# Performance work log

Hardware: AMD Instinct MI355X
Metric: run time of the kernel (lower is better)

Reference implementation:

```python
import jax, jax.numpy as jnp
from jax import lax
import numpy as np

_BN_SCALE = 1.0 / float(np.sqrt(1.0 + 1e-5))  # eval BN: running_mean=0, running_var=1
SEMANTIC_GROUPS = [
    ("head_spine", [0, 1, 2, 3, 20]),
    ("left_arm", [4, 5, 6, 7, 21, 22]),
    ("right_arm", [8, 9, 10, 11, 23, 24]),
    ("left_leg", [12, 13, 14, 15]),
    ("right_leg", [16, 17, 18, 19]),
]
_SKELETON_EDGES = [(3, 2), (2, 20), (20, 1), (1, 0), (20, 4), (4, 5), (5, 6), (6, 22), (6, 7), (7, 21),
                   (20, 8), (8, 9), (9, 10), (10, 24), (10, 11), (11, 23), (0, 12), (12, 13), (13, 14),
                   (14, 15), (0, 16), (16, 17), (17, 18), (18, 19)]


def _full_adj():
    adj = np.zeros((25, 25))
    for i, j in [(a - 1, b - 1) for a, b in _SKELETON_EDGES]:
        if 0 <= i < 25 and 0 <= j < 25:
            adj[i, j] = 1.0
            adj[j, i] = 1.0
    adj += np.eye(25)
    deg = adj.sum(1, keepdims=True)
    deg[deg == 0] = 1.0
    return adj / deg


def _sub_adj(joints):
    fa = _full_adj()
    sa = fa[np.ix_(joints, joints)].copy()
    n = len(joints)
    if n > 1:
        sa += np.eye(n)
        deg = sa.sum(1)
        for node in np.nonzero(deg == 1.0)[0]:
            if node != 0:
                sa[0, node] = 1.0
                sa[node, 0] = 1.0
    deg = sa.sum(1, keepdims=True)
    deg[deg == 0] = 1.0
    return jnp.asarray((sa / deg).astype(np.float32))


def _bn(y, g, b):
    # eval-mode BatchNorm2d with running stats (0, 1)
    return y * (g * _BN_SCALE)[None, :, None, None] + b[None, :, None, None]


def _st_layer(x, adj, sw, sb, tw, tb, g, b, res):
    # x: (B, Cin, T, V); sw: (3*Cout, Cin); tw: (Cout, Cout, 3, 1)
    if res is None:
        r = x
    else:
        rw, rb, rg, rbb = res
        r = _bn(jnp.einsum('oc,bctv->botv', rw, x) + rb[None, :, None, None], rg, rbb)
    xg = jnp.einsum('uv,bctv->bctu', adj, x)  # adjacency message passing
    y = jnp.einsum('oc,bctv->botv', sw, xg) + sb[None, :, None, None]
    B, oc3, T, V = y.shape
    y = y.reshape(B, 3, oc3 // 3, T, V).sum(axis=1)  # sum spatial kernel partitions
    y = lax.conv_general_dilated(y, tw, (1, 1), ((1, 1), (0, 0))) + tb[None, :, None, None]
    return jax.nn.relu(_bn(y + r, g, b))


def _vq(inp, cb):
    # inp: (B, D), cb: (K, D); straight-through VQ with commitment_cost=0.25
    d = jnp.sum(inp * inp, 1, keepdims=True) + jnp.sum(cb * cb, 1) - 2.0 * (inp @ cb.T)
    idx = jnp.argmin(d, axis=1)
    q = cb[idx]
    sg = lax.stop_gradient
    loss = jnp.mean((q - sg(inp)) ** 2) + 0.25 * jnp.mean((sg(q) - inp) ** 2)
    return inp + sg(q - inp), loss, idx


def _forward(x, embed_w, embed_b, p1, p2, p3, codebooks):
    h = jnp.einsum('btvc,oc->btvo', x, embed_w) + embed_b  # (B,T,25,64)
    h = h.transpose(0, 3, 1, 2)  # (B,64,T,25)
    quants, losses, idxs = [], [], []
    for gi, (_, joints) in enumerate(SEMANTIC_GROUPS):
        adj = _sub_adj(joints)
        y = h[:, :, :, np.asarray(joints)]
        sw1, sb1, tw1, tb1, g1, b1 = [p[gi] for p in p1]
        y = _st_layer(y, adj, sw1, sb1, tw1, tb1, g1, b1, None)
        rw2, rb2, rg2, rbb2, sw2, sb2, tw2, tb2, g2, b2 = [p[gi] for p in p2]
        y = _st_layer(y, adj, sw2, sb2, tw2, tb2, g2, b2, (rw2, rb2, rg2, rbb2))
        rw3, rb3, rg3, rbb3, sw3, sb3, tw3, tb3, g3, b3 = [p[gi] for p in p3]
        y = _st_layer(y, adj, sw3, sb3, tw3, tb3, g3, b3, (rw3, rb3, rg3, rbb3))
        feat = y.mean(axis=(2, 3))  # AdaptiveAvgPool2d((1,1))
        q, l, i = _vq(feat, codebooks[gi])
        quants.append(q)
        losses.append(l)
        idxs.append(i)
    return jnp.stack(quants), jnp.sum(jnp.stack(losses)), jnp.stack(idxs)


def setup_inputs() -> dict:
    ks = iter(jax.random.split(jax.random.key(0), 48))

    def rn(shape, scale=0.05):
        return jax.random.normal(next(ks), shape, jnp.float32) * scale

    return {
        "x": jax.random.normal(next(ks), (64, 256, 25, 3), jnp.float32),
        "embed_w": rn((64, 3), 0.3),
        "embed_b": rn((64,), 0.01),
        "sgcn_w1": rn((5, 192, 64)),
        "sgcn_b1": rn((5, 192), 0.01),
        "tconv_w1": rn((5, 64, 64, 3, 1)),
        "tconv_b1": rn((5, 64), 0.01),
        "bn_g1": jnp.ones((5, 64), jnp.float32),
        "bn_b1": jnp.zeros((5, 64), jnp.float32),
        "res_w2": rn((5, 128, 64)),
        "res_b2": rn((5, 128), 0.01),
        "resbn_g2": jnp.ones((5, 128), jnp.float32),
        "resbn_b2": jnp.zeros((5, 128), jnp.float32),
        "sgcn_w2": rn((5, 384, 64)),
        "sgcn_b2": rn((5, 384), 0.01),
        "tconv_w2": rn((5, 128, 128, 3, 1)),
        "tconv_b2": rn((5, 128), 0.01),
        "bn_g2": jnp.ones((5, 128), jnp.float32),
        "bn_b2": jnp.zeros((5, 128), jnp.float32),
        "res_w3": rn((5, 64, 128)),
        "res_b3": rn((5, 64), 0.01),
        "resbn_g3": jnp.ones((5, 64), jnp.float32),
        "resbn_b3": jnp.zeros((5, 64), jnp.float32),
        "sgcn_w3": rn((5, 192, 128)),
        "sgcn_b3": rn((5, 192), 0.01),
        "tconv_w3": rn((5, 64, 64, 3, 1)),
        "tconv_b3": rn((5, 64), 0.01),
        "bn_g3": jnp.ones((5, 64), jnp.float32),
        "bn_b3": jnp.zeros((5, 64), jnp.float32),
        "codebooks": jax.random.uniform(next(ks), (5, 128, 64), jnp.float32, -1.0 / 128, 1.0 / 128),
    }


def reference(x, embed_w, embed_b, sgcn_w1, sgcn_b1, tconv_w1, tconv_b1, bn_g1, bn_b1,
              res_w2, res_b2, resbn_g2, resbn_b2, sgcn_w2, sgcn_b2, tconv_w2, tconv_b2, bn_g2, bn_b2,
              res_w3, res_b3, resbn_g3, resbn_b3, sgcn_w3, sgcn_b3, tconv_w3, tconv_b3, bn_g3, bn_b3,
              codebooks):
    p1 = (sgcn_w1, sgcn_b1, tconv_w1, tconv_b1, bn_g1, bn_b1)
    p2 = (res_w2, res_b2, resbn_g2, resbn_b2, sgcn_w2, sgcn_b2, tconv_w2, tconv_b2, bn_g2, bn_b2)
    p3 = (res_w3, res_b3, resbn_g3, resbn_b3, sgcn_w3, sgcn_b3, tconv_w3, tconv_b3, bn_g3, bn_b3)
    return _forward(x, embed_w, embed_b, p1, p2, p3, codebooks)
```

## Files before the change

### kernel.cpp

```cpp
#include <hip/hip_runtime.h>

#define T_ 256
#define B_ 64
static constexpr float BNS = 0.9999950000374997f;

__device__ __constant__ int d_perm[25] = {0,1,2,3,20, 4,5,6,7,21,22, 8,9,10,11,23,24, 12,13,14,15, 16,17,18,19};
__device__ __constant__ int d_gstart[5] = {0,5,11,17,21};
__device__ __constant__ int d_gn[5] = {5,6,6,4,4};
__device__ __constant__ int d_edges[21][2] = {
  {2,1},{1,19},{19,0},{19,3},{3,4},{4,5},{5,21},{5,6},{6,20},{19,7},
  {7,8},{8,9},{9,23},{9,10},{10,22},{11,12},{12,13},{13,14},{15,16},{16,17},{17,18}};

__global__ void adj_kernel(float* __restrict__ adjout){
  if (threadIdx.x != 0 || blockIdx.x != 0) return;
  double fa[25][25];
  for (int i=0;i<25;i++) for (int j=0;j<25;j++) fa[i][j]=0.0;
  for (int e=0;e<21;e++){ int i=d_edges[e][0], j=d_edges[e][1]; fa[i][j]=1.0; fa[j][i]=1.0; }
  for (int i=0;i<25;i++) fa[i][i] += 1.0;
  for (int i=0;i<25;i++){
    double dg=0; for (int j=0;j<25;j++) dg += fa[i][j];
    if (dg==0.0) dg=1.0;
    for (int j=0;j<25;j++) fa[i][j] /= dg;
  }
  for (int g=0; g<5; g++){
    int n = d_gn[g]; int gs = d_gstart[g];
    for (int q=0;q<36;q++) adjout[g*36+q] = 0.f;
    double sa[6][6];
    for (int a=0;a<n;a++) for (int b=0;b<n;b++) sa[a][b] = fa[d_perm[gs+a]][d_perm[gs+b]];
    for (int a=0;a<n;a++) sa[a][a] += 1.0;
    double deg[6];
    for (int a=0;a<n;a++){ double s=0; for (int b=0;b<n;b++) s += sa[a][b]; deg[a]=s; }
    for (int a=1;a<n;a++) if (deg[a]==1.0){ sa[0][a]=1.0; sa[a][0]=1.0; }
    for (int a=0;a<n;a++){
      double s=0; for (int b=0;b<n;b++) s += sa[a][b];
      if (s==0.0) s=1.0;
      for (int b=0;b<n;b++) adjout[g*36 + a*n + b] = (float)(sa[a][b]/s);
    }
  }
}

__global__ void zero_kernel(float* __restrict__ feat, float* __restrict__ loss){
  int i = blockIdx.x*256 + threadIdx.x;
  if (i < 5*64*64) feat[i] = 0.f;
  if (i == 0) loss[0] = 0.f;
}

__global__ __launch_bounds__(256) void fold_swe(
    const float* __restrict__ sw1, const float* __restrict__ sw2, const float* __restrict__ sw3,
    float* __restrict__ swe1, float* __restrict__ swe2, float* __restrict__ swe3){
  int i = blockIdx.x*256 + threadIdx.x;
  if (i < 20480){ int g=i/4096, r=i%4096;
    swe1[i] = sw1[g*12288 + r] + sw1[g*12288 + 4096 + r] + sw1[g*12288 + 8192 + r];
  } else if (i < 61440){ int j=i-20480; int g=j/8192, r=j%8192;
    swe2[j] = sw2[g*24576 + r] + sw2[g*24576 + 8192 + r] + sw2[g*24576 + 16384 + r];
  } else if (i < 102400){ int j=i-61440; int g=j/8192, r=j%8192;
    swe3[j] = sw3[g*24576 + r] + sw3[g*24576 + 8192 + r] + sw3[g*24576 + 16384 + r];
  }
}

template<int Cm, int Cout>
__global__ __launch_bounds__(256) void transpose_tw(const float* __restrict__ tw, float* __restrict__ twT){
  int e = blockIdx.x*256 + threadIdx.x;
  if (e >= 5*3*Cm*Cout) return;
  int o = e % Cout;
  int t = e / Cout;
  int m = t % Cm; t /= Cm;
  int k = t % 3; int g = t/3;
  twT[e] = tw[(size_t)g*Cout*Cm*3 + (o*Cm+m)*3 + k];
}

template<int Cm, int Cin, int Cout>
__global__ __launch_bounds__(256) void prep_gemm(
    const float* __restrict__ twT, const float* __restrict__ swe,
    const float* __restrict__ bg, float* __restrict__ WC){
  constexpr int CT = 256/Cout;
  __shared__ float sS[Cm*CT];
  int g = blockIdx.x, k = blockIdx.y, cz = blockIdx.z;
  int tid = threadIdx.x;
  for (int i=tid; i<Cm*CT; i+=256){
    int m = i/CT, cc = i%CT;
    sS[i] = swe[(size_t)g*Cm*Cin + m*Cin + cz*CT + cc];
  }
  __syncthreads();
  int o = tid % Cout, cc = tid / Cout;
  const float* tp = twT + ((size_t)(g*3+k)*Cm)*Cout + o;
  float acc = 0.f;
  #pragma unroll 4
  for (int m=0;m<Cm;m++) acc += tp[(size_t)m*Cout]*sS[m*CT+cc];
  int c = cz*CT + cc;
  WC[(size_t)g*3*Cin*Cout + ((size_t)k*Cin + c)*Cout + o] = bg[g*Cout+o]*BNS*acc;
}

__global__ __launch_bounds__(256) void prep_rw(
    const float* __restrict__ rw2, const float* __restrict__ rg2, const float* __restrict__ bg2,
    const float* __restrict__ rw3, const float* __restrict__ rg3, const float* __restrict__ bg3,
    float* __restrict__ RW2, float* __restrict__ RW3){
  int i = blockIdx.x*256 + threadIdx.x;
  if (i < 40960){ int g=i/8192, r=i%8192, c=r>>7, o=r&127;
    RW2[i] = bg2[g*128+o]*BNS*rg2[g*128+o]*BNS*rw2[(size_t)g*8192 + o*64 + c];
  } else if (i < 81920){ int j=i-40960; int g=j/8192, r=j%8192, c=r>>6, o=r&63;
    RW3[j] = bg3[g*64+o]*BNS*rg3[g*64+o]*BNS*rw3[(size_t)g*8192 + o*128 + c];
  }
}

__global__ __launch_bounds__(128) void prep_bias(
    const float* __restrict__ twT1, const float* __restrict__ twT2, const float* __restrict__ twT3,
    const float* __restrict__ sb1, const float* __restrict__ tb1, const float* __restrict__ bg1, const float* __restrict__ bb1,
    const float* __restrict__ sb2, const float* __restrict__ tb2, const float* __restrict__ bg2, const float* __restrict__ bb2,
    const float* __restrict__ rb2, const float* __restrict__ rg2, const float* __restrict__ rbb2,
    const float* __restrict__ sb3, const float* __restrict__ tb3, const float* __restrict__ bg3, const float* __restrict__ bb3,
    const float* __restrict__ rb3, const float* __restrict__ rg3, const float* __restrict__ rbb3,
    float* __restrict__ B1, float* __restrict__ RS1, float* __restrict__ B2, float* __restrict__ B3){
  __shared__ float sbe[128];
  int g = blockIdx.x, L = blockIdx.y, tid = threadIdx.x;
  if (L == 0){
    if (tid<64) sbe[tid] = sb1[g*192+tid] + sb1[g*192+64+tid] + sb1[g*192+128+tid];
    __syncthreads();
    if (tid<64){ int o=tid; float gsc = bg1[g*64+o]*BNS;
      for (int k=0;k<3;k++){ float s=0.f; const float* tp = twT1 + ((size_t)(g*3+k)*64)*64 + o;
        for (int m=0;m<64;m++) s += tp[m*64]*sbe[m];
        B1[g*256+(k+1)*64+o] = gsc*s; }
      B1[g*256+o] = gsc*tb1[g*64+o] + bb1[g*64+o];
      RS1[g*64+o] = gsc;
    }
  } else if (L == 1){
    sbe[tid] = sb2[g*384+tid] + sb2[g*384+128+tid] + sb2[g*384+256+tid];
    __syncthreads();
    { int o=tid; float gsc = bg2[g*128+o]*BNS; float rgs = rg2[g*128+o]*BNS;
      for (int k=0;k<3;k++){ float s=0.f; const float* tp = twT2 + ((size_t)(g*3+k)*128)*128 + o;
        for (int m=0;m<128;m++) s += tp[m*128]*sbe[m];
        B2[g*512+(k+1)*128+o] = gsc*s; }
      B2[g*512+o] = gsc*(tb2[g*128+o] + rgs*rb2[g*128+o] + rbb2[g*128+o]) + bb2[g*128+o];
    }
  } else {
    if (tid<64) sbe[tid] = sb3[g*192+tid] + sb3[g*192+64+tid] + sb3[g*192+128+tid];
    __syncthreads();
    if (tid<64){ int o=tid; float gsc = bg3[g*64+o]*BNS; float rgs = rg3[g*64+o]*BNS;
      for (int k=0;k<3;k++){ float s=0.f; const float* tp = twT3 + ((size_t)(g*3+k)*64)*64 + o;
        for (int m=0;m<64;m++) s += tp[m*64]*sbe[m];
        B3[g*256+(k+1)*64+o] = gsc*s; }
      B3[g*256+o] = gsc*(tb3[g*64+o] + rgs*rb3[g*64+o] + rbb3[g*64+o]) + bb3[g*64+o];
    }
  }
}

template<int Cin, int COS, int NJ, int MODE>
__global__ __launch_bounds__(256, 4) void st_layer(
    const float* __restrict__ in, float* __restrict__ out,
    const float* __restrict__ W, const float* __restrict__ RW,
    const float* __restrict__ BV, const float* __restrict__ RS,
    const float* __restrict__ adjg, const float* __restrict__ ew,
    const float* __restrict__ eb, int gstart)
{
  constexpr int TC = 16;
  constexpr int SE = (TC+2)*NJ;
  constexpr int SITES = TC*NJ;
  constexpr int SP = SITES/8;
  constexpr int OP = 2;
  constexpr int NCH = Cin/32;
  __shared__ float sIn[SE*32];
  __shared__ float sXg[SE*32];
  __shared__ float sAdj[NJ*NJ];
  __shared__ float sX3[MODE==1 ? SE*3 : 1];
  const int tid = threadIdx.x;
  const int b = blockIdx.y;
  const int t0 = blockIdx.x*TC;
  const int ooff = blockIdx.z*64;
  W += ooff; BV += ooff;
  if (MODE != 1) RW += ooff;
  if (MODE == 2) out += ooff;

  if (tid < NJ*NJ) sAdj[tid] = adjg[tid];
  if (MODE == 1){
    for (int e=tid; e<SE*3; e+=256){
      int se = e/3, j = e - se*3;
      int tl = se/NJ; int u = se - tl*NJ; int t = t0 + tl - 1;
      float v = 0.f;
      if (t>=0 && t<T_){ int joint = d_perm[gstart+u]; v = in[(((size_t)b*T_ + t)*25 + joint)*3 + j]; }
      sX3[e] = v;
    }
  }

  const int lane = tid & 63;
  const int o = lane & 31;
  const int sg = (tid>>6)*2 + (lane>>5);
  const int s0 = sg*SP;

  float acc[SP][OP];
  {
    float bno[OP], bk0[OP], bk1[OP], bk2[OP];
    #pragma unroll
    for (int j=0;j<OP;j++){ int oj = j*32 + o;
      bno[j]=BV[oj]; bk0[j]=BV[COS+oj]; bk1[j]=BV[2*COS+oj]; bk2[j]=BV[3*COS+oj]; }
    #pragma unroll
    for (int i=0;i<SP;i++){
      int s = s0 + i; int tg = t0 + s/NJ;
      #pragma unroll
      for (int j=0;j<OP;j++)
        acc[i][j] = bno[j] + bk1[j] + (tg>0 ? bk0[j] : 0.f) + (tg<T_-1 ? bk2[j] : 0.f);
    }
  }

  #pragma unroll 1
  for (int cz=0; cz<NCH; ++cz){
    __syncthreads();
    if (MODE == 1){
      int cg = cz*32 + (tid & 31);
      float w0 = ew[cg*3], w1 = ew[cg*3+1], w2 = ew[cg*3+2], b0 = eb[cg];
      for (int e=tid; e<SE*32; e+=256){
        int se = e>>5; int t = t0 + se/NJ - 1;
        float v = 0.f;
        if (t>=0 && t<T_) v = b0 + sX3[se*3]*w0 + sX3[se*3+1]*w1 + sX3[se*3+2]*w2;
        sIn[e] = v;
      }
    } else {
      for (int e4=tid; e4<SE*8; e4+=256){
        int se = e4>>3; int cc = (e4&7)<<2;
        int tl = se/NJ; int u = se - tl*NJ; int t = t0 + tl - 1;
        float4 v = make_float4(0.f,0.f,0.f,0.f);
        if (t>=0 && t<T_) v = *(const float4*)&in[(((size_t)b*T_ + t)*NJ + u)*(size_t)Cin + cz*32 + cc];
        *(float4*)&sIn[se*32+cc] = v;
      }
    }
    __syncthreads();
    for (int e=tid; e<SE*32; e+=256){
      int se = e>>5; int c = e&31; int u = se%NJ; int base = (se-u)*32 + c;
      float a = 0.f;
      #pragma unroll
      for (int v=0; v<NJ; v++) a += sAdj[u*NJ+v]*sIn[base + v*32];
      sXg[e] = a;
    }
    __syncthreads();
    #pragma unroll 1
    for (int k=0;k<3;k++){
      const float* Wk = W + (size_t)(k*Cin + cz*32)*COS;
      #pragma unroll 2
      for (int c4=0;c4<32;c4+=4){
        float wv[4][OP];
        #pragma unroll
        for (int q=0;q<4;q++)
          #pragma unroll
          for (int j=0;j<OP;j++) wv[q][j] = Wk[(size_t)(c4+q)*COS + j*32 + o];
        #pragma unroll
        for (int i=0;i<SP;i++){
          const float4 xv = *(const float4*)&sXg[(s0+i+k*NJ)*32 + c4];
          #pragma unroll
          for (int j=0;j<OP;j++)
            acc[i][j] += xv.x*wv[0][j] + xv.y*wv[1][j] + xv.z*wv[2][j] + xv.w*wv[3][j];
        }
      }
    }
    if (MODE == 1){
      float rsv = RS[cz*32 + o];
      #pragma unroll
      for (int i=0;i<SP;i++)
        acc[i][cz] += sIn[(s0+i+NJ)*32 + o]*rsv;
    } else {
      #pragma unroll 2
      for (int c4=0;c4<32;c4+=4){
        float rv[4][OP];
        #pragma unroll
        for (int q=0;q<4;q++)
          #pragma unroll
          for (int j=0;j<OP;j++) rv[q][j] = RW[(size_t)(cz*32+c4+q)*COS + j*32 + o];
        #pragma unroll
        for (int i=0;i<SP;i++){
          const float4 xv = *(const float4*)&sIn[(s0+i+NJ)*32 + c4];
          #pragma unroll
          for (int j=0;j<OP;j++)
            acc[i][j] += xv.x*rv[0][j] + xv.y*rv[1][j] + xv.z*rv[2][j] + xv.w*rv[3][j];
        }
      }
    }
  }
  if (MODE == 3){
    #pragma unroll
    for (int j=0;j<OP;j++){
      float sum = 0.f;
      #pragma unroll
      for (int i=0;i<SP;i++) sum += fmaxf(acc[i][j], 0.f);
      atomicAdd(&out[(size_t)b*64 + j*32 + o], sum);
    }
  } else {
    size_t obase = ((size_t)b*T_ + t0)*NJ*COS;
    #pragma unroll
    for (int i=0;i<SP;i++)
      #pragma unroll
      for (int j=0;j<OP;j++)
        out[obase + (size_t)(s0+i)*COS + j*32 + o] = fmaxf(acc[i][j], 0.f);
  }
}

__global__ __launch_bounds__(128) void vq_kernel(const float* __restrict__ feat,
    const float* __restrict__ cb, float* __restrict__ dout){
  int b = blockIdx.x, g = blockIdx.y, tid = threadIdx.x;
  __shared__ float sF[64];
  __shared__ float sD[128]; __shared__ int sI[128];
  __shared__ float sL[64];
  float inv = 1.0f/(256.0f*(float)d_gn[g]);
  if (tid < 64) sF[tid] = feat[((size_t)g*64 + b)*64 + tid]*inv;
  __syncthreads();
  const float* cbg = cb + (size_t)g*128*64;
  {
    const float* c = cbg + (size_t)tid*64;
    float d = 0.f;
    for (int i=0;i<64;i++){ float df = c[i]-sF[i]; d += df*df; }
    sD[tid] = d; sI[tid] = tid;
  }
  __syncthreads();
  for (int s=64; s>0; s>>=1){
    if (tid < s){
      float d2 = sD[tid+s]; int i2 = sI[tid+s];
      if (d2 < sD[tid] || (d2 == sD[tid] && i2 < sI[tid])){ sD[tid]=d2; sI[tid]=i2; }
    }
    __syncthreads();
  }
  int idx = sI[0];
  if (tid < 64){
    float q = cbg[(size_t)idx*64 + tid];
    dout[((size_t)g*64 + b)*64 + tid] = q;
    float df = q - sF[tid];
    sL[tid] = df*df;
  }
  __syncthreads();
  if (tid == 0){
    float s = 0.f;
    for (int i=0;i<64;i++) s += sL[i];
    atomicAdd(dout + 20480, 1.25f*s/4096.0f);
    dout[20481 + g*64 + b] = (float)idx;
  }
}

static void launch_st1(int nj, hipStream_t s, const float* x, float* A1,
    const float* WC, const float* BV, const float* RS, const float* adj,
    const float* ew, const float* eb, int gstart){
  dim3 grid(T_/16, B_, 1);
  switch(nj){
    case 4: st_layer<64,64,4,1><<<grid,256,0,s>>>(x,A1,WC,nullptr,BV,RS,adj,ew,eb,gstart); break;
    case 5: st_layer<64,64,5,1><<<grid,256,0,s>>>(x,A1,WC,nullptr,BV,RS,adj,ew,eb,gstart); break;
    case 6: st_layer<64,64,6,1><<<grid,256,0,s>>>(x,A1,WC,nullptr,BV,RS,adj,ew,eb,gstart); break;
  }
}
static void launch_st2(int nj, hipStream_t s, const float* A1, float* A2,
    const float* WC, const float* RW, const float* BV, const float* adj){
  dim3 grid(T_/16, B_, 2);
  switch(nj){
    case 4: st_layer<64,128,4,2><<<grid,256,0,s>>>(A1,A2,WC,RW,BV,nullptr,adj,nullptr,nullptr,0); break;
    case 5: st_layer<64,128,5,2><<<grid,256,0,s>>>(A1,A2,WC,RW,BV,nullptr,adj,nullptr,nullptr,0); break;
    case 6: st_layer<64,128,6,2><<<grid,256,0,s>>>(A1,A2,WC,RW,BV,nullptr,adj,nullptr,nullptr,0); break;
  }
}
static void launch_st3(int nj, hipStream_t s, const float* A2, float* featg,
    const float* WC, const float* RW, const float* BV, const float* adj){
  dim3 grid(T_/16, B_, 1);
  switch(nj){
    case 4: st_layer<128,64,4,3><<<grid,256,0,s>>>(A2,featg,WC,RW,BV,nullptr,adj,nullptr,nullptr,0); break;
    case 5: st_layer<128,64,5,3><<<grid,256,0,s>>>(A2,featg,WC,RW,BV,nullptr,adj,nullptr,nullptr,0); break;
    case 6: st_layer<128,64,6,3><<<grid,256,0,s>>>(A2,featg,WC,RW,BV,nullptr,adj,nullptr,nullptr,0); break;
  }
}

extern "C" void kernel_launch(void* const* d_in, const int* in_sizes, int n_in,
                              void* d_out, int out_size, void* d_ws, size_t ws_size,
                              hipStream_t stream) {
  const float* x    = (const float*)d_in[0];
  const float* ew   = (const float*)d_in[1];
  const float* eb   = (const float*)d_in[2];
  const float* sw1  = (const float*)d_in[3];
  const float* sb1  = (const float*)d_in[4];
  const float* tw1  = (const float*)d_in[5];
  const float* tb1  = (const float*)d_in[6];
  const float* bg1  = (const float*)d_in[7];
  const float* bb1  = (const float*)d_in[8];
  const float* rw2  = (const float*)d_in[9];
  const float* rb2  = (const float*)d_in[10];
  const float* rg2  = (const float*)d_in[11];
  const float* rbb2 = (const float*)d_in[12];
  const float* sw2  = (const float*)d_in[13];
  const float* sb2  = (const float*)d_in[14];
  const float* tw2  = (const float*)d_in[15];
  const float* tb2  = (const float*)d_in[16];
  const float* bg2  = (const float*)d_in[17];
  const float* bb2  = (const float*)d_in[18];
  const float* rw3  = (const float*)d_in[19];
  const float* rb3  = (const float*)d_in[20];
  const float* rg3  = (const float*)d_in[21];
  const float* rbb3 = (const float*)d_in[22];
  const float* sw3  = (const float*)d_in[23];
  const float* sb3  = (const float*)d_in[24];
  const float* tw3  = (const float*)d_in[25];
  const float* tb3  = (const float*)d_in[26];
  const float* bg3  = (const float*)d_in[27];
  const float* bb3  = (const float*)d_in[28];
  const float* cbs  = (const float*)d_in[29];
  float* dout = (float*)d_out;
  float* ws = (float*)d_ws;

  const size_t OFF_ADJ = 0;
  const size_t OFF_WC1 = 256;
  const size_t OFF_B1  = 61696;
  const size_t OFF_RS1 = 62976;
  const size_t OFF_WC2 = 63296;
  const size_t OFF_RW2 = 186176;
  const size_t OFF_B2  = 227136;
  const size_t OFF_WC3 = 229696;
  const size_t OFF_RW3 = 352576;
  const size_t OFF_B3  = 393536;
  const size_t OFF_FEAT= 394816;
  const size_t OFF_A1  = 415296;
  const size_t OFF_A2  = 6706752;
  const size_t WS_FLOATS = 19289664;
  if (ws_size < WS_FLOATS*sizeof(float)) return;

  float* adj5 = ws + OFF_ADJ;
  float* WC1  = ws + OFF_WC1;  float* B1 = ws + OFF_B1;  float* RS1 = ws + OFF_RS1;
  float* WC2  = ws + OFF_WC2;  float* RW2 = ws + OFF_RW2; float* B2 = ws + OFF_B2;
  float* WC3  = ws + OFF_WC3;  float* RW3 = ws + OFF_RW3; float* B3 = ws + OFF_B3;
  float* feat = ws + OFF_FEAT;
  float* A1   = ws + OFF_A1;
  float* A2   = ws + OFF_A2;

  float* twT1 = A2;
  float* twT2 = A2 + 61440;
  float* twT3 = A2 + 307200;
  float* swe1 = A2 + 368640;
  float* swe2 = A2 + 389120;
  float* swe3 = A2 + 430080;

  zero_kernel<<<80, 256, 0, stream>>>(feat, dout + 20480);
  adj_kernel<<<1, 64, 0, stream>>>(adj5);
  fold_swe<<<400, 256, 0, stream>>>(sw1, sw2, sw3, swe1, swe2, swe3);
  transpose_tw<64,64>  <<<240, 256, 0, stream>>>(tw1, twT1);
  transpose_tw<128,128><<<960, 256, 0, stream>>>(tw2, twT2);
  transpose_tw<64,64>  <<<240, 256, 0, stream>>>(tw3, twT3);
  prep_gemm<64,64,64>  <<<dim3(5,3,16), 256, 0, stream>>>(twT1, swe1, bg1, WC1);
  prep_gemm<128,64,128><<<dim3(5,3,32), 256, 0, stream>>>(twT2, swe2, bg2, WC2);
  prep_gemm<64,128,64> <<<dim3(5,3,32), 256, 0, stream>>>(twT3, swe3, bg3, WC3);
  prep_rw<<<320, 256, 0, stream>>>(rw2, rg2, bg2, rw3, rg3, bg3, RW2, RW3);
  prep_bias<<<dim3(5,3), 128, 0, stream>>>(twT1, twT2, twT3,
      sb1, tb1, bg1, bb1,
      sb2, tb2, bg2, bb2, rb2, rg2, rbb2,
      sb3, tb3, bg3, bb3, rb3, rg3, rbb3,
      B1, RS1, B2, B3);

  const int h_gn[5] = {5,6,6,4,4};
  const int h_gstart[5] = {0,5,11,17,21};
  for (int g=0; g<5; g++){
    int nj = h_gn[g];
    launch_st1(nj, stream, x, A1, WC1 + (size_t)g*12288, B1 + g*256, RS1 + g*64,
               adj5 + g*36, ew, eb, h_gstart[g]);
    launch_st2(nj, stream, A1, A2, WC2 + (size_t)g*24576, RW2 + (size_t)g*8192,
               B2 + g*512, adj5 + g*36);
    launch_st3(nj, stream, A2, feat + (size_t)g*4096, WC3 + (size_t)g*24576,
               RW3 + (size_t)g*8192, B3 + g*256, adj5 + g*36);
  }
  vq_kernel<<<dim3(B_,5), 128, 0, stream>>>(feat, cbs, dout);
}
```

Baseline: 1.712 ms.

## Retile st_layer thread mapping to 16x16 and pad shared rows

Changes the register tile of the ST-GCN layer kernel from 32 outputs x 2 site groups per wavefront to 16 output lanes x 16 site groups, with each thread holding 4 output channels and half as many sites. Shared-memory rows are padded from 32 to 36 floats so the float4 reads from different sites land in different banks. The occupancy hint in launch bounds is removed so the compiler may use more registers. Each thread now reuses each shared-memory activation across 4 outputs, which cuts LDS traffic, but the weight loads become 16-wide and occupancy may drop.

```diff
diff --git a/kernel.cpp b/kernel.cpp
--- a/kernel.cpp
+++ b/kernel.cpp
@@ -145,7 +145,7 @@
 }
 
 template<int Cin, int COS, int NJ, int MODE>
-__global__ __launch_bounds__(256, 4) void st_layer(
+__global__ __launch_bounds__(256) void st_layer(
     const float* __restrict__ in, float* __restrict__ out,
     const float* __restrict__ W, const float* __restrict__ RW,
     const float* __restrict__ BV, const float* __restrict__ RS,
@@ -155,11 +155,12 @@
   constexpr int TC = 16;
   constexpr int SE = (TC+2)*NJ;
   constexpr int SITES = TC*NJ;
-  constexpr int SP = SITES/8;
-  constexpr int OP = 2;
+  constexpr int SP = SITES/16;
+  constexpr int OP = 4;
   constexpr int NCH = Cin/32;
-  __shared__ float sIn[SE*32];
-  __shared__ float sXg[SE*32];
+  constexpr int RST = 36;
+  __shared__ float sIn[SE*RST];
+  __shared__ float sXg[SE*RST];
   __shared__ float sAdj[NJ*NJ];
   __shared__ float sX3[MODE==1 ? SE*3 : 1];
   const int tid = threadIdx.x;
@@ -181,16 +182,15 @@
     }
   }
 
-  const int lane = tid & 63;
-  const int o = lane & 31;
-  const int sg = (tid>>6)*2 + (lane>>5);
+  const int o = tid & 15;
+  const int sg = tid >> 4;
   const int s0 = sg*SP;
 
   float acc[SP][OP];
   {
     float bno[OP], bk0[OP], bk1[OP], bk2[OP];
     #pragma unroll
-    for (int j=0;j<OP;j++){ int oj = j*32 + o;
+    for (int j=0;j<OP;j++){ int oj = j*16 + o;
       bno[j]=BV[oj]; bk0[j]=BV[COS+oj]; bk1[j]=BV[2*COS+oj]; bk2[j]=BV[3*COS+oj]; }
     #pragma unroll
     for (int i=0;i<SP;i++){
@@ -208,10 +208,10 @@
       int cg = cz*32 + (tid & 31);
       float w0 = ew[cg*3], w1 = ew[cg*3+1], w2 = ew[cg*3+2], b0 = eb[cg];
       for (int e=tid; e<SE*32; e+=256){
-        int se = e>>5; int t = t0 + se/NJ - 1;
+        int se = e>>5; int c = e&31; int t = t0 + se/NJ - 1;
         float v = 0.f;
         if (t>=0 && t<T_) v = b0 + sX3[se*3]*w0 + sX3[se*3+1]*w1 + sX3[se*3+2]*w2;
-        sIn[e] = v;
+        sIn[se*RST + c] = v;
       }
     } else {
       for (int e4=tid; e4<SE*8; e4+=256){
@@ -219,16 +219,16 @@
         int tl = se/NJ; int u = se - tl*NJ; int t = t0 + tl - 1;
         float4 v = make_float4(0.f,0.f,0.f,0.f);
         if (t>=0 && t<T_) v = *(const float4*)&in[(((size_t)b*T_ + t)*NJ + u)*(size_t)Cin + cz*32 + cc];
-        *(float4*)&sIn[se*32+cc] = v;
+        *(float4*)&sIn[se*RST+cc] = v;
       }
     }
     __syncthreads();
     for (int e=tid; e<SE*32; e+=256){
-      int se = e>>5; int c = e&31; int u = se%NJ; int base = (se-u)*32 + c;
+      int se = e>>5; int c = e&31; int u = se%NJ; int base = (se-u)*RST + c;
       float a = 0.f;
       #pragma unroll
-      for (int v=0; v<NJ; v++) a += sAdj[u*NJ+v]*sIn[base + v*32];
-      sXg[e] = a;
+      for (int v=0; v<NJ; v++) a += sAdj[u*NJ+v]*sIn[base + v*RST];
+      sXg[se*RST + c] = a;
     }
     __syncthreads();
     #pragma unroll 1
@@ -240,10 +240,10 @@
         #pragma unroll
         for (int q=0;q<4;q++)
           #pragma unroll
-          for (int j=0;j<OP;j++) wv[q][j] = Wk[(size_t)(c4+q)*COS + j*32 + o];
+          for (int j=0;j<OP;j++) wv[q][j] = Wk[(size_t)(c4+q)*COS + j*16 + o];
         #pragma unroll
         for (int i=0;i<SP;i++){
-          const float4 xv = *(const float4*)&sXg[(s0+i+k*NJ)*32 + c4];
+          const float4 xv = *(const float4*)&sXg[(s0+i+k*NJ)*RST + c4];
           #pragma unroll
           for (int j=0;j<OP;j++)
             acc[i][j] += xv.x*wv[0][j] + xv.y*wv[1][j] + xv.z*wv[2][j] + xv.w*wv[3][j];
@@ -251,10 +251,21 @@
       }
     }
     if (MODE == 1){
-      float rsv = RS[cz*32 + o];
-      #pragma unroll
-      for (int i=0;i<SP;i++)
-        acc[i][cz] += sIn[(s0+i+NJ)*32 + o]*rsv;
+      if (cz == 0){
+        float r0 = RS[o], r1 = RS[16+o];
+        #pragma unroll
+        for (int i=0;i<SP;i++){
+          acc[i][0] += sIn[(s0+i+NJ)*RST + o]*r0;
+          acc[i][1] += sIn[(s0+i+NJ)*RST + 16 + o]*r1;
+        }
+      } else {
+        float r2 = RS[32+o], r3 = RS[48+o];
+        #pragma unroll
+        for (int i=0;i<SP;i++){
+          acc[i][2] += sIn[(s0+i+NJ)*RST + o]*r2;
+          acc[i][3] += sIn[(s0+i+NJ)*RST + 16 + o]*r3;
+        }
+      }
     } else {
       #pragma unroll 2
       for (int c4=0;c4<32;c4+=4){
@@ -262,10 +273,10 @@
         #pragma unroll
         for (int q=0;q<4;q++)
           #pragma unroll
-          for (int j=0;j<OP;j++) rv[q][j] = RW[(size_t)(cz*32+c4+q)*COS + j*32 + o];
+          for (int j=0;j<OP;j++) rv[q][j] = RW[(size_t)(cz*32+c4+q)*COS + j*16 + o];
         #pragma unroll
         for (int i=0;i<SP;i++){
-          const float4 xv = *(const float4*)&sIn[(s0+i+NJ)*32 + c4];
+          const float4 xv = *(const float4*)&sIn[(s0+i+NJ)*RST + c4];
           #pragma unroll
           for (int j=0;j<OP;j++)
             acc[i][j] += xv.x*rv[0][j] + xv.y*rv[1][j] + xv.z*rv[2][j] + xv.w*rv[3][j];
@@ -279,7 +290,7 @@
       float sum = 0.f;
       #pragma unroll
       for (int i=0;i<SP;i++) sum += fmaxf(acc[i][j], 0.f);
-      atomicAdd(&out[(size_t)b*64 + j*32 + o], sum);
+      atomicAdd(&out[(size_t)b*64 + j*16 + o], sum);
     }
   } else {
     size_t obase = ((size_t)b*T_ + t0)*NJ*COS;
@@ -287,7 +298,7 @@
     for (int i=0;i<SP;i++)
       #pragma unroll
       for (int j=0;j<OP;j++)
-        out[obase + (size_t)(s0+i)*COS + j*32 + o] = fmaxf(acc[i][j], 0.f);
+        out[obase + (size_t)(s0+i)*COS + j*16 + o] = fmaxf(acc[i][j], 0.f);
   }
 }
 
```

Result: faster. 1.660 ms (-3.0%).
